# Optimization experiments

Measured on AMD Instinct MI355X. Metric: run time of the kernel, lower is better.

Reference implementation:

```python
import jax, jax.numpy as jnp
import numpy as np
import math

EMBED = 1024
HEADS = 16
HEAD_DIM = EMBED // HEADS
FFN = 4 * EMBED
LAYERS = 3
SEQ = 2048
BATCH = 2
INPUT_DIM = 64


def make_pe(max_len, d_model):
    pe = np.zeros((max_len, d_model), dtype=np.float32)
    pos = np.arange(max_len, dtype=np.float32)[:, None]
    div = np.exp(np.arange(0, d_model, 2, dtype=np.float32) * (-math.log(10000.0) / d_model))
    pe[:, 0::2] = np.sin(pos * div)
    pe[:, 1::2] = np.cos(pos * div)
    return jnp.asarray(pe)


def setup_inputs() -> dict:
    key = jax.random.key(0)
    ks = jax.random.split(key, 16)
    s = lambda k, shape, fan: jax.random.normal(k, shape, dtype=jnp.float32) / np.sqrt(fan)
    return {
        "x": jax.random.normal(ks[0], (BATCH, SEQ, INPUT_DIM), dtype=jnp.float32),
        "mask": jnp.ones((BATCH, 1, 1, SEQ), dtype=bool),
        "embed_W": s(ks[1], (INPUT_DIM, EMBED), INPUT_DIM),
        "embed_b": jnp.zeros((EMBED,), jnp.float32),
        "pe": make_pe(SEQ, EMBED),
        "Wq": s(ks[2], (LAYERS, HEAD_DIM, HEAD_DIM), HEAD_DIM),
        "Wk": s(ks[3], (LAYERS, HEAD_DIM, HEAD_DIM), HEAD_DIM),
        "Wv": s(ks[4], (LAYERS, HEAD_DIM, HEAD_DIM), HEAD_DIM),
        "Wo": s(ks[5], (LAYERS, EMBED, EMBED), EMBED),
        "bo": jnp.zeros((LAYERS, EMBED), jnp.float32),
        "ln1_g": jnp.ones((LAYERS, EMBED), jnp.float32),
        "ln1_b": jnp.zeros((LAYERS, EMBED), jnp.float32),
        "W1": s(ks[6], (LAYERS, EMBED, FFN), EMBED),
        "b1": jnp.zeros((LAYERS, FFN), jnp.float32),
        "W2": s(ks[7], (LAYERS, FFN, EMBED), FFN),
        "b2": jnp.zeros((LAYERS, EMBED), jnp.float32),
        "ln2_g": jnp.ones((LAYERS, EMBED), jnp.float32),
        "ln2_b": jnp.zeros((LAYERS, EMBED), jnp.float32),
    }


def _layernorm(x, g, b, eps=1e-5):
    mu = jnp.mean(x, axis=-1, keepdims=True)
    var = jnp.var(x, axis=-1, keepdims=True)
    return (x - mu) * jax.lax.rsqrt(var + eps) * g + b


def reference(x, mask, embed_W, embed_b, pe, Wq, Wk, Wv, Wo, bo,
              ln1_g, ln1_b, W1, b1, W2, b2, ln2_g, ln2_b):
    N, S, _ = x.shape
    scale = 1.0 / np.sqrt(EMBED).astype(np.float32)  # note: sqrt(embed_size), as in original
    h = x @ embed_W + embed_b + pe[None, :S, :]
    for l in range(LAYERS):
        hr = h.reshape(N, S, HEADS, HEAD_DIM)
        q = jnp.einsum('nshd,de->nshe', hr, Wq[l])
        k = jnp.einsum('nshd,de->nshe', hr, Wk[l])
        v = jnp.einsum('nshd,de->nshe', hr, Wv[l])
        energy = jnp.einsum('nqhd,nkhd->nhqk', q, k)  # (N,H,S,S)
        energy = jnp.where(mask == 0, jnp.float32(-1e20), energy)
        attn = jax.nn.softmax(energy * scale, axis=-1)
        o = jnp.einsum('nhqk,nkhd->nqhd', attn, v).reshape(N, S, EMBED)
        o = o @ Wo[l] + bo[l]
        x1 = _layernorm(o + h, ln1_g[l], ln1_b[l])
        ff = jax.nn.relu(x1 @ W1[l] + b1[l]) @ W2[l] + b2[l]
        h = _layernorm(ff + x1, ln2_g[l], ln2_b[l])
    return h
```

## Files before the change

kernel.cpp:

```cpp
#include <hip/hip_runtime.h>


typedef __attribute__((ext_vector_type(8))) unsigned short us8;
typedef __attribute__((ext_vector_type(4))) unsigned short us4;
typedef __attribute__((ext_vector_type(8))) __bf16 bf16x8;
typedef __attribute__((ext_vector_type(4))) float f32x4;

#define SEQ   2048
#define HEADS 16
#define HD    64
#define EMB   1024
#define FFN_  4096
#define NBAT  2
#define ROWS  (NBAT*SEQ)

__device__ __forceinline__ float bf2f(unsigned short s) {
    return __builtin_bit_cast(float, ((unsigned int)s) << 16);
}
__device__ __forceinline__ unsigned short f2bf(float f) {
    unsigned int u = __builtin_bit_cast(unsigned int, f);
    u += 0x7fffu + ((u >> 16) & 1u);
    return (unsigned short)(u >> 16);
}
__device__ __forceinline__ bf16x8 ldfrag(const unsigned short* p) {
    us8 v = *(const us8*)p;
    return __builtin_bit_cast(bf16x8, v);
}
__device__ __forceinline__ us8 cvt8(const float* p) {
    float4 f0 = *(const float4*)p, f1 = *(const float4*)(p + 4);
    us8 v;
    v[0] = f2bf(f0.x); v[1] = f2bf(f0.y); v[2] = f2bf(f0.z); v[3] = f2bf(f0.w);
    v[4] = f2bf(f1.x); v[5] = f2bf(f1.y); v[6] = f2bf(f1.z); v[7] = f2bf(f1.w);
    return v;
}
__device__ __forceinline__ void async_cp16(const unsigned short* g, unsigned short* l) {
    __builtin_amdgcn_global_load_lds(
        (const __attribute__((address_space(1))) void*)g,
        (__attribute__((address_space(3))) void*)l, 16, 0, 0);
}

__device__ __forceinline__ void transpose_tile(
    const float* __restrict__ W, unsigned short* __restrict__ Wt,
    int K, int N, int k0, int n0, int t)
{
    __shared__ float T[64][65];
    const int kk = t >> 4, nn = (t & 15) * 4;
#pragma unroll
    for (int r = 0; r < 4; r++) {
        float4 v = *(const float4*)(W + (size_t)(k0 + kk + r*16)*N + n0 + nn);
        T[kk + r*16][nn+0] = v.x; T[kk + r*16][nn+1] = v.y;
        T[kk + r*16][nn+2] = v.z; T[kk + r*16][nn+3] = v.w;
    }
    __syncthreads();
    const int n = t >> 2, kc = (t & 3) * 16;
    us8 a, b;
#pragma unroll
    for (int i = 0; i < 8; i++) a[i] = f2bf(T[kc + i][n]);
#pragma unroll
    for (int i = 0; i < 8; i++) b[i] = f2bf(T[kc + 8 + i][n]);
    *(us8*)(Wt + (size_t)(n0 + n)*K + k0 + kc)     = a;
    *(us8*)(Wt + (size_t)(n0 + n)*K + k0 + kc + 8) = b;
}

__global__ __launch_bounds__(256) void wprep(
    const float* __restrict__ W, unsigned short* __restrict__ Wt,
    const int K, const int N)
{
    transpose_tile(W, Wt, K, N, blockIdx.x*64, blockIdx.y*64, threadIdx.x);
}

__global__ __launch_bounds__(256) void wprep_qkv(
    const float* __restrict__ Wq, const float* __restrict__ Wk,
    const float* __restrict__ Wv, unsigned short* __restrict__ Wt3)
{
    const float* W = blockIdx.z == 0 ? Wq : (blockIdx.z == 1 ? Wk : Wv);
    transpose_tile(W, Wt3 + (size_t)blockIdx.z*64*64, 64, 64, 0, 0, threadIdx.x);
}

__global__ __launch_bounds__(256) void cvt_bf16(
    const float* __restrict__ src, unsigned short* __restrict__ dst, const int n8)
{
    int i = blockIdx.x*256 + threadIdx.x;
    if (i < n8) *(us8*)(dst + (size_t)i*8) = cvt8(src + (size_t)i*8);
}

__global__ __launch_bounds__(256) void vtrans(
    const unsigned short* __restrict__ QKV, unsigned short* __restrict__ Vt)
{
    __shared__ __align__(16) unsigned short T[64*72];
    const int s0 = blockIdx.x*64, h = blockIdx.y, n = blockIdx.z;
    const int t = threadIdx.x;
    const int s = t & 63, c16 = (t >> 6) * 16;
    const unsigned short* src =
        QKV + ((size_t)(n*SEQ + s0 + s)*HEADS + h)*192 + 128 + c16;
    *(us8*)&T[s*72 + c16]     = *(const us8*)(src);
    *(us8*)&T[s*72 + c16 + 8] = *(const us8*)(src + 8);
    __syncthreads();
    const int f = t & 63, r16 = (t >> 6) * 16;
    us8 a, b;
#pragma unroll
    for (int i = 0; i < 8; i++) a[i] = T[(r16 + i)*72 + f];
#pragma unroll
    for (int i = 0; i < 8; i++) b[i] = T[(r16 + 8 + i)*72 + f];
    unsigned short* dst = Vt + ((size_t)(n*HEADS + h)*HD + f)*SEQ + s0 + r16;
    *(us8*)dst       = a;
    *(us8*)(dst + 8) = b;
}

template<int BM, int BN, int WR, int WC>
__global__ __launch_bounds__(WR*WC*64) void gemm_bt(
    const unsigned short* __restrict__ A, const unsigned short* __restrict__ Bt,
    void* __restrict__ Cout, const int out_bf16,
    const float* __restrict__ bias, const float* __restrict__ pe,
    const int M, const int N, const int K, const int relu)
{
    constexpr int BK  = 32;
    constexpr int NW  = WR*WC;
    constexpr int MF  = BM/(WR*16);
    constexpr int NF  = BN/(WC*16);
    constexpr int ACH = BM*4;
    constexpr int BCH = BN*4;
    constexpr int APW = ACH/NW;
    constexpr int BPW = BCH/NW;
    __shared__ __align__(16) unsigned short As[BM*BK];
    __shared__ __align__(16) unsigned short Bs[BN*BK];

    const int tid  = threadIdx.x;
    const int lane = tid & 63;
    const int wave = tid >> 6;
    const int wm   = (wave / WC) * (BM/WR);
    const int wn   = (wave % WC) * (BN/WC);
    const int bm   = blockIdx.x * BM;
    const int bn   = blockIdx.y * BN;
    const int m15  = lane & 15;
    const int quad = lane >> 4;

    f32x4 acc[MF][NF];
#pragma unroll
    for (int i = 0; i < MF; i++)
#pragma unroll
        for (int j = 0; j < NF; j++) acc[i][j] = (f32x4){0.f, 0.f, 0.f, 0.f};

    for (int kt = 0; kt < K; kt += BK) {
#pragma unroll
        for (int j = 0; j < APW/64; j++) {
            const int c = wave*APW + j*64 + lane;
            async_cp16(A + (size_t)(bm + (c >> 2))*K + kt + (c & 3)*8,
                       As + (size_t)(wave*APW + j*64)*8);
        }
#pragma unroll
        for (int j = 0; j < BPW/64; j++) {
            const int c = wave*BPW + j*64 + lane;
            async_cp16(Bt + (size_t)(bn + (c >> 2))*K + kt + (c & 3)*8,
                       Bs + (size_t)(wave*BPW + j*64)*8);
        }
        __syncthreads();

        bf16x8 af[MF], bfr[NF];
#pragma unroll
        for (int i = 0; i < MF; i++) af[i]  = ldfrag(&As[(wm + i*16 + m15)*BK + quad*8]);
#pragma unroll
        for (int j = 0; j < NF; j++) bfr[j] = ldfrag(&Bs[(wn + j*16 + m15)*BK + quad*8]);
#pragma unroll
        for (int i = 0; i < MF; i++)
#pragma unroll
            for (int j = 0; j < NF; j++)
                acc[i][j] = __builtin_amdgcn_mfma_f32_16x16x32_bf16(af[i], bfr[j], acc[i][j], 0, 0, 0);
        __syncthreads();
    }

#pragma unroll
    for (int i = 0; i < MF; i++) {
#pragma unroll
        for (int j = 0; j < NF; j++) {
#pragma unroll
            for (int r = 0; r < 4; r++) {
                int row = bm + wm + i*16 + quad*4 + r;
                int col = bn + wn + j*16 + m15;
                float v = acc[i][j][r];
                if (bias) v += bias[col];
                if (pe)   v += pe[(size_t)(row & (SEQ-1))*EMB + col];
                if (relu) v = fmaxf(v, 0.f);
                if (out_bf16) ((unsigned short*)Cout)[(size_t)row*N + col] = f2bf(v);
                else          ((float*)Cout)[(size_t)row*N + col] = v;
            }
        }
    }
}

__global__ __launch_bounds__(256) void flash_attn(
    const unsigned short* __restrict__ QKV, const unsigned short* __restrict__ Vt,
    unsigned short* __restrict__ O)
{
    const int h = blockIdx.y, n = blockIdx.z;
    const int tid = threadIdx.x, lane = tid & 63, wave = tid >> 6;
    const int m15 = lane & 15, quad = lane >> 4;
    const int q0 = blockIdx.x*128 + wave*32;

    __shared__ __align__(16) unsigned short Ks[2][64*64];
    __shared__ __align__(16) unsigned short Vs[2][64*64];
    __shared__ __align__(16) unsigned short Pl[4][32*36];

    bf16x8 aq[2][2];
#pragma unroll
    for (int mi = 0; mi < 2; mi++) {
        const unsigned short* qp =
            QKV + ((size_t)(n*SEQ + q0 + mi*16 + m15)*HEADS + h)*192;
        aq[mi][0] = ldfrag(qp + quad*8);
        aq[mi][1] = ldfrag(qp + 32 + quad*8);
    }

    f32x4 accO[2][4];
    f32x4 lacc[2];
#pragma unroll
    for (int mi = 0; mi < 2; mi++) {
        lacc[mi] = (f32x4){0.f, 0.f, 0.f, 0.f};
#pragma unroll
        for (int ft = 0; ft < 4; ft++) accO[mi][ft] = (f32x4){0.f, 0.f, 0.f, 0.f};
    }

    const float sl2e = 0.03125f * 1.4426950408889634f;
    const unsigned short* kb = QKV + ((size_t)(n*SEQ)*HEADS + h)*192 + 64;
    const unsigned short* vb = Vt + (size_t)(n*HEADS + h)*HD*SEQ;

    us8 ones_u;
#pragma unroll
    for (int i = 0; i < 8; i++) ones_u[i] = 0x3F80;
    const bf16x8 ones = __builtin_bit_cast(bf16x8, ones_u);

    const int r0  = tid >> 3;
    const int r1  = r0 + 32;
    const int sc  = ((tid & 7) ^ (r0 & 7)) * 8;
    const int swz = (m15 & 7);

    auto stage = [&](int buf, int kt) {
        async_cp16(kb + (size_t)(kt + r0)*(HEADS*192) + sc, Ks[buf] + (size_t)(wave*64)*8);
        async_cp16(kb + (size_t)(kt + r1)*(HEADS*192) + sc, Ks[buf] + (size_t)(256 + wave*64)*8);
        async_cp16(vb + (size_t)r0*SEQ + kt + sc,           Vs[buf] + (size_t)(wave*64)*8);
        async_cp16(vb + (size_t)r1*SEQ + kt + sc,           Vs[buf] + (size_t)(256 + wave*64)*8);
    };

    stage(0, 0);
    __syncthreads();
    int cur = 0;

    for (int kt = 0; kt < SEQ; kt += 64) {
        stage(cur ^ 1, (kt + 64) & (SEQ - 1));
        const unsigned short* ksp = Ks[cur];
        const unsigned short* vsp = Vs[cur];

#pragma unroll
        for (int s2 = 0; s2 < 2; s2++) {
            bf16x8 ck[2][2], cv[4];
#pragma unroll
            for (int nt = 0; nt < 2; nt++)
#pragma unroll
                for (int ks = 0; ks < 2; ks++) {
                    const int kk = s2*32 + nt*16 + m15;
                    ck[nt][ks] = ldfrag(&ksp[kk*64 + (((ks*4 + quad) ^ swz) * 8)]);
                }
#pragma unroll
            for (int ft = 0; ft < 4; ft++) {
                const int d = ft*16 + m15;
                cv[ft] = ldfrag(&vsp[d*64 + (((s2*4 + quad) ^ swz) * 8)]);
            }

            f32x4 sv[2][2];
            __builtin_amdgcn_s_setprio(1);
#pragma unroll
            for (int mi = 0; mi < 2; mi++)
#pragma unroll
                for (int nt = 0; nt < 2; nt++) {
                    f32x4 z = (f32x4){0.f, 0.f, 0.f, 0.f};
                    z = __builtin_amdgcn_mfma_f32_16x16x32_bf16(aq[mi][0], ck[nt][0], z, 0, 0, 0);
                    z = __builtin_amdgcn_mfma_f32_16x16x32_bf16(aq[mi][1], ck[nt][1], z, 0, 0, 0);
                    sv[mi][nt] = z;
                }
            __builtin_amdgcn_s_setprio(0);

#pragma unroll
            for (int mi = 0; mi < 2; mi++)
#pragma unroll
                for (int nt = 0; nt < 2; nt++)
#pragma unroll
                    for (int r = 0; r < 4; r += 2) {
                        float p0 = exp2f(fminf(sv[mi][nt][r]   * sl2e, 80.f));
                        float p1 = exp2f(fminf(sv[mi][nt][r+1] * sl2e, 80.f));
                        unsigned int pk;
                        asm("v_cvt_pk_bf16_f32 %0, %1, %2"
                            : "=v"(pk) : "v"(p0), "v"(p1));
                        Pl[wave][(mi*16 + quad*4 + r    )*36 + nt*16 + m15] =
                            (unsigned short)(pk & 0xffffu);
                        Pl[wave][(mi*16 + quad*4 + r + 1)*36 + nt*16 + m15] =
                            (unsigned short)(pk >> 16);
                    }

            bf16x8 pf[2];
#pragma unroll
            for (int mi = 0; mi < 2; mi++)
                pf[mi] = ldfrag(&Pl[wave][(mi*16 + m15)*36 + quad*8]);
            __builtin_amdgcn_s_setprio(1);
#pragma unroll
            for (int mi = 0; mi < 2; mi++) {
#pragma unroll
                for (int ft = 0; ft < 4; ft++)
                    accO[mi][ft] = __builtin_amdgcn_mfma_f32_16x16x32_bf16(
                        pf[mi], cv[ft], accO[mi][ft], 0, 0, 0);
                lacc[mi] = __builtin_amdgcn_mfma_f32_16x16x32_bf16(
                    pf[mi], ones, lacc[mi], 0, 0, 0);
            }
            __builtin_amdgcn_s_setprio(0);
        }

        __syncthreads();
        cur ^= 1;
    }

#pragma unroll
    for (int mi = 0; mi < 2; mi++)
#pragma unroll
        for (int r = 0; r < 4; r++) {
            const float inv = 1.0f / lacc[mi][r];
            const int row = q0 + mi*16 + quad*4 + r;
#pragma unroll
            for (int ft = 0; ft < 4; ft++)
                O[((size_t)(n*SEQ + row)*HEADS + h)*HD + ft*16 + m15] =
                    f2bf(accO[mi][ft][r] * inv);
        }
}

__global__ __launch_bounds__(256) void add_ln_kernel(
    const unsigned short* __restrict__ a, const unsigned short* __restrict__ res,
    const float* __restrict__ g, const float* __restrict__ b,
    void* __restrict__ out, const int out_fp32)
{
    const int row = blockIdx.x;
    const int tid = threadIdx.x;
    const int c0  = tid * 4;

    us4 va = *(const us4*)(a   + (size_t)row*EMB + c0);
    us4 vr = *(const us4*)(res + (size_t)row*EMB + c0);
    float x[4];
#pragma unroll
    for (int i = 0; i < 4; i++) x[i] = bf2f(va[i]) + bf2f(vr[i]);

    float s = x[0] + x[1] + x[2] + x[3];
    float q = x[0]*x[0] + x[1]*x[1] + x[2]*x[2] + x[3]*x[3];
#pragma unroll
    for (int off = 1; off < 64; off <<= 1) {
        s += __shfl_xor(s, off, 64);
        q += __shfl_xor(q, off, 64);
    }
    __shared__ float rs[4], rq[4];
    if ((tid & 63) == 0) { rs[tid >> 6] = s; rq[tid >> 6] = q; }
    __syncthreads();
    s = rs[0] + rs[1] + rs[2] + rs[3];
    q = rq[0] + rq[1] + rq[2] + rq[3];

    const float mu   = s * (1.0f/EMB);
    const float var  = q * (1.0f/EMB) - mu*mu;
    const float rstd = rsqrtf(var + 1e-5f);

    float4 vg = *(const float4*)(g + c0);
    float4 vb = *(const float4*)(b + c0);
    float y0 = (x[0] - mu) * rstd * vg.x + vb.x;
    float y1 = (x[1] - mu) * rstd * vg.y + vb.y;
    float y2 = (x[2] - mu) * rstd * vg.z + vb.z;
    float y3 = (x[3] - mu) * rstd * vg.w + vb.w;

    if (out_fp32) {
        *(float4*)((float*)out + (size_t)row*EMB + c0) = (float4){y0, y1, y2, y3};
    } else {
        us4 o;
        o[0] = f2bf(y0); o[1] = f2bf(y1); o[2] = f2bf(y2); o[3] = f2bf(y3);
        *(us4*)((unsigned short*)out + (size_t)row*EMB + c0) = o;
    }
}

extern "C" void kernel_launch(void* const* d_in, const int* in_sizes, int n_in,
                              void* d_out, int out_size, void* d_ws, size_t ws_size,
                              hipStream_t stream)
{
    (void)in_sizes; (void)n_in; (void)out_size; (void)ws_size;
    const float* x    = (const float*)d_in[0];
    const float* embW = (const float*)d_in[2];
    const float* embB = (const float*)d_in[3];
    const float* pe   = (const float*)d_in[4];
    const float* Wq   = (const float*)d_in[5];
    const float* Wk   = (const float*)d_in[6];
    const float* Wv   = (const float*)d_in[7];
    const float* Wo   = (const float*)d_in[8];
    const float* bo   = (const float*)d_in[9];
    const float* ln1g = (const float*)d_in[10];
    const float* ln1b = (const float*)d_in[11];
    const float* W1   = (const float*)d_in[12];
    const float* b1   = (const float*)d_in[13];
    const float* W2   = (const float*)d_in[14];
    const float* b2   = (const float*)d_in[15];
    const float* ln2g = (const float*)d_in[16];
    const float* ln2b = (const float*)d_in[17];

    char* ws = (char*)d_ws;
    const size_t MB = 1024*1024;
    unsigned short* qkv = (unsigned short*)ws;
    unsigned short* ff  = (unsigned short*)ws;
    unsigned short* vt  = (unsigned short*)(ws + 24*MB);
    unsigned short* t   = (unsigned short*)(ws + 32*MB);
    unsigned short* h   = (unsigned short*)(ws + 40*MB);
    unsigned short* x1  = (unsigned short*)(ws + 48*MB);
    unsigned short* wx  = (unsigned short*)(ws + 56*MB);
    unsigned short* xb    = t;
    unsigned short* embWt = t + 256*1024;
    unsigned short* qkvWt = t;
    unsigned short* o   = (unsigned short*)d_out;

    cvt_bf16<<<128, 256, 0, stream>>>(x, xb, ROWS*64/8);
    wprep<<<dim3(1, EMB/64), 256, 0, stream>>>(embW, embWt, 64, EMB);
    gemm_bt<128,64,4,1><<<dim3(ROWS/128, EMB/64), 256, 0, stream>>>(
        xb, embWt, h, 1, embB, pe, ROWS, EMB, 64, 0);

    for (int l = 0; l < 3; l++) {
        wprep_qkv<<<dim3(1,1,3), 256, 0, stream>>>(
            Wq + (size_t)l*HD*HD, Wk + (size_t)l*HD*HD, Wv + (size_t)l*HD*HD, qkvWt);
        gemm_bt<256,64,4,1><<<dim3(ROWS*HEADS/256, 3), 256, 0, stream>>>(
            h, qkvWt, qkv, 1, nullptr, nullptr, ROWS*HEADS, 192, HD, 0);

        vtrans<<<dim3(SEQ/64, HEADS, NBAT), 256, 0, stream>>>(qkv, vt);
        flash_attn<<<dim3(SEQ/128, HEADS, NBAT), 256, 0, stream>>>(qkv, vt, o);

        wprep<<<dim3(EMB/64, EMB/64), 256, 0, stream>>>(
            Wo + (size_t)l*EMB*EMB, wx, EMB, EMB);
        gemm_bt<128,64,4,1><<<dim3(ROWS/128, EMB/64), 256, 0, stream>>>(
            o, wx, t, 1, bo + (size_t)l*EMB, nullptr, ROWS, EMB, EMB, 0);
        add_ln_kernel<<<ROWS, 256, 0, stream>>>(
            t, h, ln1g + (size_t)l*EMB, ln1b + (size_t)l*EMB, x1, 0);

        wprep<<<dim3(EMB/64, FFN_/64), 256, 0, stream>>>(
            W1 + (size_t)l*EMB*FFN_, wx, EMB, FFN_);
        gemm_bt<128,128,2,2><<<dim3(ROWS/128, FFN_/128), 256, 0, stream>>>(
            x1, wx, ff, 1, b1 + (size_t)l*FFN_, nullptr, ROWS, FFN_, EMB, 1);
        wprep<<<dim3(FFN_/64, EMB/64), 256, 0, stream>>>(
            W2 + (size_t)l*FFN_*EMB, wx, FFN_, EMB);
        gemm_bt<128,64,4,1><<<dim3(ROWS/128, EMB/64), 256, 0, stream>>>(
            ff, wx, t, 1, b2 + (size_t)l*EMB, nullptr, ROWS, EMB, FFN_, 0);

        if (l == 2)
            add_ln_kernel<<<ROWS, 256, 0, stream>>>(
                t, x1, ln2g + (size_t)l*EMB, ln2b + (size_t)l*EMB, d_out, 1);
        else
            add_ln_kernel<<<ROWS, 256, 0, stream>>>(
                t, x1, ln2g + (size_t)l*EMB, ln2b + (size_t)l*EMB, h, 0);
    }
}
```

Before: 1.130 ms.

## Compute transposed attention scores to keep P in registers, dropping LDS round-trip

The flash attention inner loop now computes S^T (K as the A operand, Q as B), so each lane's score accumulator already matches the B-operand layout of the 16x16x16 bf16 MFMA. P can then be packed straight into registers and fed to the PV product as O^T = V^T P^T, with no LDS write/read of P. This removes the per-wave P scratch buffer and its stores, loads and bank traffic. In exchange it uses more, smaller K=16 MFMAs for PV and the row-sum, and it changes the V fragment reads and the output store pattern.

```diff
diff --git a/kernel.cpp b/kernel.cpp
--- a/kernel.cpp
+++ b/kernel.cpp
@@ -5,6 +5,8 @@
 typedef __attribute__((ext_vector_type(4))) unsigned short us4;
 typedef __attribute__((ext_vector_type(8))) __bf16 bf16x8;
 typedef __attribute__((ext_vector_type(4))) float f32x4;
+typedef __attribute__((ext_vector_type(4))) short sh4;
+typedef __attribute__((ext_vector_type(2))) unsigned int u32x2;
 
 #define SEQ   2048
 #define HEADS 16
@@ -25,6 +27,9 @@
 __device__ __forceinline__ bf16x8 ldfrag(const unsigned short* p) {
     us8 v = *(const us8*)p;
     return __builtin_bit_cast(bf16x8, v);
+}
+__device__ __forceinline__ f32x4 mfma16(sh4 a, sh4 b, f32x4 c) {
+    return __builtin_amdgcn_mfma_f32_16x16x16bf16_1k(a, b, c, 0, 0, 0);
 }
 __device__ __forceinline__ us8 cvt8(const float* p) {
     float4 f0 = *(const float4*)p, f1 = *(const float4*)(p + 4);
@@ -199,7 +204,6 @@
 
     __shared__ __align__(16) unsigned short Ks[2][64*64];
     __shared__ __align__(16) unsigned short Vs[2][64*64];
-    __shared__ __align__(16) unsigned short Pl[4][32*36];
 
     bf16x8 aq[2][2];
 #pragma unroll
@@ -220,13 +224,13 @@
     }
 
     const float sl2e = 0.03125f * 1.4426950408889634f;
-    const unsigned short* kb = QKV + ((size_t)(n*SEQ)*HEADS + h)*192 + 64;
-    const unsigned short* vb = Vt + (size_t)(n*HEADS + h)*HD*SEQ;
-
-    us8 ones_u;
-#pragma unroll
-    for (int i = 0; i < 8; i++) ones_u[i] = 0x3F80;
-    const bf16x8 ones = __builtin_bit_cast(bf16x8, ones_u);
+    const unsigned short* kb_ = QKV + ((size_t)(n*SEQ)*HEADS + h)*192 + 64;
+    const unsigned short* vb  = Vt + (size_t)(n*HEADS + h)*HD*SEQ;
+
+    us4 ones_u;
+#pragma unroll
+    for (int i = 0; i < 4; i++) ones_u[i] = 0x3F80;
+    const sh4 ones4 = __builtin_bit_cast(sh4, ones_u);
 
     const int r0  = tid >> 3;
     const int r1  = r0 + 32;
@@ -234,10 +238,10 @@
     const int swz = (m15 & 7);
 
     auto stage = [&](int buf, int kt) {
-        async_cp16(kb + (size_t)(kt + r0)*(HEADS*192) + sc, Ks[buf] + (size_t)(wave*64)*8);
-        async_cp16(kb + (size_t)(kt + r1)*(HEADS*192) + sc, Ks[buf] + (size_t)(256 + wave*64)*8);
-        async_cp16(vb + (size_t)r0*SEQ + kt + sc,           Vs[buf] + (size_t)(wave*64)*8);
-        async_cp16(vb + (size_t)r1*SEQ + kt + sc,           Vs[buf] + (size_t)(256 + wave*64)*8);
+        async_cp16(kb_ + (size_t)(kt + r0)*(HEADS*192) + sc, Ks[buf] + (size_t)(wave*64)*8);
+        async_cp16(kb_ + (size_t)(kt + r1)*(HEADS*192) + sc, Ks[buf] + (size_t)(256 + wave*64)*8);
+        async_cp16(vb + (size_t)r0*SEQ + kt + sc,            Vs[buf] + (size_t)(wave*64)*8);
+        async_cp16(vb + (size_t)r1*SEQ + kt + sc,            Vs[buf] + (size_t)(256 + wave*64)*8);
     };
 
     stage(0, 0);
@@ -250,66 +254,49 @@
         const unsigned short* vsp = Vs[cur];
 
 #pragma unroll
-        for (int s2 = 0; s2 < 2; s2++) {
-            bf16x8 ck[2][2], cv[4];
-#pragma unroll
-            for (int nt = 0; nt < 2; nt++)
-#pragma unroll
-                for (int ks = 0; ks < 2; ks++) {
-                    const int kk = s2*32 + nt*16 + m15;
-                    ck[nt][ks] = ldfrag(&ksp[kk*64 + (((ks*4 + quad) ^ swz) * 8)]);
-                }
-#pragma unroll
-            for (int ft = 0; ft < 4; ft++) {
-                const int d = ft*16 + m15;
-                cv[ft] = ldfrag(&vsp[d*64 + (((s2*4 + quad) ^ swz) * 8)]);
-            }
-
-            f32x4 sv[2][2];
+        for (int kb = 0; kb < 4; kb++) {
+            bf16x8 ckf[2];
+#pragma unroll
+            for (int ks = 0; ks < 2; ks++)
+                ckf[ks] = ldfrag(&ksp[(kb*16 + m15)*64 + (((ks*4 + quad) ^ swz) * 8)]);
+
+            f32x4 st[2];
             __builtin_amdgcn_s_setprio(1);
 #pragma unroll
-            for (int mi = 0; mi < 2; mi++)
-#pragma unroll
-                for (int nt = 0; nt < 2; nt++) {
-                    f32x4 z = (f32x4){0.f, 0.f, 0.f, 0.f};
-                    z = __builtin_amdgcn_mfma_f32_16x16x32_bf16(aq[mi][0], ck[nt][0], z, 0, 0, 0);
-                    z = __builtin_amdgcn_mfma_f32_16x16x32_bf16(aq[mi][1], ck[nt][1], z, 0, 0, 0);
-                    sv[mi][nt] = z;
-                }
-            __builtin_amdgcn_s_setprio(0);
-
-#pragma unroll
-            for (int mi = 0; mi < 2; mi++)
-#pragma unroll
-                for (int nt = 0; nt < 2; nt++)
-#pragma unroll
-                    for (int r = 0; r < 4; r += 2) {
-                        float p0 = exp2f(fminf(sv[mi][nt][r]   * sl2e, 80.f));
-                        float p1 = exp2f(fminf(sv[mi][nt][r+1] * sl2e, 80.f));
-                        unsigned int pk;
-                        asm("v_cvt_pk_bf16_f32 %0, %1, %2"
-                            : "=v"(pk) : "v"(p0), "v"(p1));
-                        Pl[wave][(mi*16 + quad*4 + r    )*36 + nt*16 + m15] =
-                            (unsigned short)(pk & 0xffffu);
-                        Pl[wave][(mi*16 + quad*4 + r + 1)*36 + nt*16 + m15] =
-                            (unsigned short)(pk >> 16);
-                    }
-
-            bf16x8 pf[2];
-#pragma unroll
-            for (int mi = 0; mi < 2; mi++)
-                pf[mi] = ldfrag(&Pl[wave][(mi*16 + m15)*36 + quad*8]);
-            __builtin_amdgcn_s_setprio(1);
-#pragma unroll
             for (int mi = 0; mi < 2; mi++) {
-#pragma unroll
-                for (int ft = 0; ft < 4; ft++)
-                    accO[mi][ft] = __builtin_amdgcn_mfma_f32_16x16x32_bf16(
-                        pf[mi], cv[ft], accO[mi][ft], 0, 0, 0);
-                lacc[mi] = __builtin_amdgcn_mfma_f32_16x16x32_bf16(
-                    pf[mi], ones, lacc[mi], 0, 0, 0);
+                f32x4 z = (f32x4){0.f, 0.f, 0.f, 0.f};
+                z = __builtin_amdgcn_mfma_f32_16x16x32_bf16(ckf[0], aq[mi][0], z, 0, 0, 0);
+                z = __builtin_amdgcn_mfma_f32_16x16x32_bf16(ckf[1], aq[mi][1], z, 0, 0, 0);
+                st[mi] = z;
             }
             __builtin_amdgcn_s_setprio(0);
+
+            sh4 pf[2];
+#pragma unroll
+            for (int mi = 0; mi < 2; mi++) {
+                float p0 = exp2f(fminf(st[mi][0] * sl2e, 80.f));
+                float p1 = exp2f(fminf(st[mi][1] * sl2e, 80.f));
+                float p2 = exp2f(fminf(st[mi][2] * sl2e, 80.f));
+                float p3 = exp2f(fminf(st[mi][3] * sl2e, 80.f));
+                unsigned int a, b;
+                asm("v_cvt_pk_bf16_f32 %0, %1, %2" : "=v"(a) : "v"(p0), "v"(p1));
+                asm("v_cvt_pk_bf16_f32 %0, %1, %2" : "=v"(b) : "v"(p2), "v"(p3));
+                u32x2 pp; pp[0] = a; pp[1] = b;
+                pf[mi] = __builtin_bit_cast(sh4, pp);
+            }
+
+            __builtin_amdgcn_s_setprio(1);
+#pragma unroll
+            for (int ft = 0; ft < 4; ft++) {
+                const int d  = ft*16 + m15;
+                const int ch = (kb*2 + (quad >> 1)) ^ (d & 7);
+                sh4 vf = *(const sh4*)&vsp[d*64 + ch*8 + (quad & 1)*4];
+                accO[0][ft] = mfma16(vf, pf[0], accO[0][ft]);
+                accO[1][ft] = mfma16(vf, pf[1], accO[1][ft]);
+            }
+            lacc[0] = mfma16(ones4, pf[0], lacc[0]);
+            lacc[1] = mfma16(ones4, pf[1], lacc[1]);
+            __builtin_amdgcn_s_setprio(0);
         }
 
         __syncthreads();
@@ -317,16 +304,18 @@
     }
 
 #pragma unroll
-    for (int mi = 0; mi < 2; mi++)
-#pragma unroll
-        for (int r = 0; r < 4; r++) {
-            const float inv = 1.0f / lacc[mi][r];
-            const int row = q0 + mi*16 + quad*4 + r;
-#pragma unroll
-            for (int ft = 0; ft < 4; ft++)
-                O[((size_t)(n*SEQ + row)*HEADS + h)*HD + ft*16 + m15] =
-                    f2bf(accO[mi][ft][r] * inv);
+    for (int mi = 0; mi < 2; mi++) {
+        const int q = q0 + mi*16 + m15;
+        const float inv = 1.0f / lacc[mi][0];
+        unsigned short* op = O + ((size_t)(n*SEQ + q)*HEADS + h)*HD;
+#pragma unroll
+        for (int ft = 0; ft < 4; ft++) {
+            us4 o4;
+#pragma unroll
+            for (int r = 0; r < 4; r++) o4[r] = f2bf(accO[mi][ft][r] * inv);
+            *(us4*)(op + ft*16 + quad*4) = o4;
         }
+    }
 }
 
 __global__ __launch_bounds__(256) void add_ln_kernel(
```

Result: faster. 1.093 ms (-3.3%).
